# Performance work log

Measured on AMD Instinct MI355X. Metric: run time of the kernel, lower is better.

Reference implementation:

```python
import jax, jax.numpy as jnp
import numpy as np

B, N, C, H, E, K = 2, 2048, 1024, 4096, 8, 2
TAU = 1.0


def setup_inputs() -> dict:
    key = jax.random.key(0)
    ks = jax.random.split(key, 9)
    x = jax.random.normal(ks[0], (B, N, C), dtype=jnp.float32)
    T = B * N
    u = jax.random.uniform(ks[1], (T, E), minval=1e-6, maxval=1.0 - 1e-6)
    gumbel_noise = -jnp.log(-jnp.log(u))  # Gumbel(0,1) samples
    s = 0.02
    gate_w = jax.random.normal(ks[2], (C, E), dtype=jnp.float32) * s
    gate_b = jnp.zeros((E,), dtype=jnp.float32)
    w1 = jax.random.normal(ks[3], (E, C, H), dtype=jnp.float32) * s
    b1 = jnp.zeros((E, H), dtype=jnp.float32)
    w2 = jax.random.normal(ks[4], (E, H, C), dtype=jnp.float32) * s
    b2 = jnp.zeros((E, C), dtype=jnp.float32)
    return {"x": x, "gumbel_noise": gumbel_noise, "gate_w": gate_w,
            "gate_b": gate_b, "w1": w1, "b1": b1, "w2": w2, "b2": b2}


def reference(x, gumbel_noise, gate_w, gate_b, w1, b1, w2, b2):
    Bb, Nn, Cc = x.shape
    x_flat = x.reshape(-1, Cc)                                  # [T, C]
    logits = x_flat @ gate_w + gate_b                           # [T, E]
    # F.gumbel_softmax(hard=False, tau=1): softmax((logits + g)/tau)
    gates = jax.nn.softmax((logits + gumbel_noise) / TAU, axis=-1)
    mean_gates = gates.mean(axis=0)
    load_balance_loss = jnp.sum(mean_gates * jnp.log(mean_gates + 1e-8))
    topk_vals, topk_idxs = jax.lax.top_k(gates, K)              # [T, K]
    T = x_flat.shape[0]
    # scatter top-k gate weights into a dense [T, E] combine matrix
    comb = jnp.zeros((T, E), dtype=gates.dtype)
    comb = comb.at[jnp.arange(T)[:, None], topk_idxs].set(topk_vals)
    # dense per-expert MLP over all tokens, then weighted combine
    h = jnp.einsum('tc,ech->teh', x_flat, w1) + b1              # [T, E, H]
    h = jax.nn.gelu(h, approximate=False)                        # exact GELU (nn.GELU)
    y = jnp.einsum('teh,ehc->tec', h, w2) + b2                  # [T, E, C]
    out = jnp.einsum('te,tec->tc', comb, y)                     # [T, C]
    return out.reshape(Bb, Nn, Cc), load_balance_loss
```

## Files before the change

kernel.cpp:

```cpp
#include <hip/hip_runtime.h>
#include <math.h>

#define TT  4096
#define CC  1024
#define HH  4096
#define EE  8
#define TKN 8192

typedef _Float16 f16x8 __attribute__((ext_vector_type(8)));
typedef float    f32x4 __attribute__((ext_vector_type(4)));

#define GLD_LDS16(g, l)                                                        \
    __builtin_amdgcn_global_load_lds(                                          \
        (const __attribute__((address_space(1))) void*)(g),                    \
        (__attribute__((address_space(3))) void*)(l), 16, 0, 0)

__global__ __launch_bounds__(256) void gate_kernel(
    const float* __restrict__ x, const float* __restrict__ gn,
    const float* __restrict__ gw, const float* __restrict__ gb,
    int* __restrict__ topk_idx, float* __restrict__ topk_w,
    int* __restrict__ counts, float* __restrict__ gsum)
{
    int wave = threadIdx.x >> 6, lane = threadIdx.x & 63;
    int t = blockIdx.x * 4 + wave;
    const float* xrow = x + (size_t)t * CC;

    double acc[EE];
#pragma unroll
    for (int e = 0; e < EE; e++) acc[e] = 0.0;

#pragma unroll
    for (int i = 0; i < CC / 64; i++) {
        int c = i * 64 + lane;
        float xv = xrow[c];
        const float4* g4 = reinterpret_cast<const float4*>(gw + (size_t)c * EE);
        float4 g0 = g4[0], g1 = g4[1];
        double xd = (double)xv;
        acc[0] += xd * (double)g0.x; acc[1] += xd * (double)g0.y;
        acc[2] += xd * (double)g0.z; acc[3] += xd * (double)g0.w;
        acc[4] += xd * (double)g1.x; acc[5] += xd * (double)g1.y;
        acc[6] += xd * (double)g1.z; acc[7] += xd * (double)g1.w;
    }
#pragma unroll
    for (int e = 0; e < EE; e++)
#pragma unroll
        for (int off = 32; off > 0; off >>= 1)
            acc[e] += __shfl_xor(acc[e], off);

    double z[EE], m = -1e300;
#pragma unroll
    for (int e = 0; e < EE; e++) {
        z[e] = acc[e] + (double)gb[e] + (double)gn[(size_t)t * EE + e];
        m = fmax(m, z[e]);
    }
    double p[EE], s = 0.0;
#pragma unroll
    for (int e = 0; e < EE; e++) { p[e] = exp(z[e] - m); s += p[e]; }
    double inv = 1.0 / s;
    double g[EE];
#pragma unroll
    for (int e = 0; e < EE; e++) g[e] = p[e] * inv;

    int i1 = 0; double v1 = g[0];
#pragma unroll
    for (int e = 1; e < EE; e++) if (g[e] > v1) { v1 = g[e]; i1 = e; }
    int i2 = -1; double v2 = -1.0;
#pragma unroll
    for (int e = 0; e < EE; e++) if (e != i1 && g[e] > v2) { v2 = g[e]; i2 = e; }

    if (lane == 0) {
        topk_idx[t * 2 + 0] = i1; topk_w[t * 2 + 0] = (float)v1;
        topk_idx[t * 2 + 1] = i2; topk_w[t * 2 + 1] = (float)v2;
        atomicAdd(&counts[i1], 1);
        atomicAdd(&counts[i2], 1);
    }

    __shared__ float gp[4][EE];
    if (lane == 0) {
#pragma unroll
        for (int e = 0; e < EE; e++) gp[wave][e] = (float)g[e];
    }
    __syncthreads();
    if (threadIdx.x < EE) {
        float s4 = gp[0][threadIdx.x] + gp[1][threadIdx.x] +
                   gp[2][threadIdx.x] + gp[3][threadIdx.x];
        atomicAdd(&gsum[threadIdx.x], s4);
    }
}

__global__ __launch_bounds__(256) void transpose_f16_kernel(
    const float* __restrict__ src, _Float16* __restrict__ dst, int R, int Ccols)
{
    __shared__ float tile[64][65];
    int e = blockIdx.z;
    const float* s = src + (size_t)e * R * Ccols;
    _Float16* d = dst + (size_t)e * R * Ccols;
    int c0 = blockIdx.x * 64, r0 = blockIdx.y * 64;
    int tx = threadIdx.x, ty = threadIdx.y;
#pragma unroll
    for (int i = 0; i < 16; i++) {
        int r = ty + i * 4;
        tile[r][tx] = s[(size_t)(r0 + r) * Ccols + c0 + tx];
    }
    __syncthreads();
#pragma unroll
    for (int i = 0; i < 16; i++) {
        int c = ty + i * 4;
        d[(size_t)(c0 + c) * R + r0 + tx] = (_Float16)tile[tx][c];
    }
}

__global__ void scan_kernel(const int* __restrict__ counts, int* __restrict__ offsets,
                            const float* __restrict__ gsum, float* __restrict__ loss_out)
{
    if (threadIdx.x == 0) {
        int o = 0;
#pragma unroll
        for (int e = 0; e < EE; e++) { offsets[e] = o; o += counts[e]; }
        offsets[EE] = o;
        float L = 0.f;
#pragma unroll
        for (int e = 0; e < EE; e++) {
            float me = gsum[e] / (float)TT;
            L += me * logf(me + 1e-8f);
        }
        *loss_out = L;
    }
}

__global__ __launch_bounds__(256) void scatter_kernel(
    const int* __restrict__ topk_idx, const float* __restrict__ topk_w,
    const int* __restrict__ offsets, int* __restrict__ fill,
    int* __restrict__ rowtok, float* __restrict__ rweight)
{
    int t = blockIdx.x * 256 + threadIdx.x;
#pragma unroll
    for (int k = 0; k < 2; k++) {
        int e = topk_idx[t * 2 + k];
        int pos = offsets[e] + atomicAdd(&fill[e], 1);
        rowtok[pos] = t;
        rweight[pos] = topk_w[t * 2 + k];
    }
}

__global__ __launch_bounds__(256) void gather_kernel(
    const float* __restrict__ x, const int* __restrict__ rowtok,
    _Float16* __restrict__ xg)
{
    int p = blockIdx.x * 2 + (threadIdx.x >> 7);
    int c = (threadIdx.x & 127) * 8;
    int t = rowtok[p];
    const float4* s = reinterpret_cast<const float4*>(x + (size_t)t * CC + c);
    float4 v0 = s[0], v1 = s[1];
    f16x8 o;
    o[0] = (_Float16)v0.x; o[1] = (_Float16)v0.y;
    o[2] = (_Float16)v0.z; o[3] = (_Float16)v0.w;
    o[4] = (_Float16)v1.x; o[5] = (_Float16)v1.y;
    o[6] = (_Float16)v1.z; o[7] = (_Float16)v1.w;
    *reinterpret_cast<f16x8*>(xg + (size_t)p * CC + c) = o;
}

__global__ __launch_bounds__(256) void gemm1_kernel(
    const _Float16* __restrict__ xg, const _Float16* __restrict__ w1t,
    const float* __restrict__ b1, const int* __restrict__ offsets,
    _Float16* __restrict__ h)
{
    int e = blockIdx.z;
    int segs = offsets[e];
    int M = offsets[e + 1] - segs;
    int m0 = blockIdx.x * 128;
    if (m0 >= M) return;
    int n0 = blockIdx.y * 128;

    __shared__ __align__(16) _Float16 As[128][64];
    __shared__ __align__(16) _Float16 Bs[128][64];

    int tid = threadIdx.x;
    int wave = tid >> 6, lane = tid & 63;
    int wm = (wave >> 1) * 64, wn = (wave & 1) * 64;
    int lrow = lane & 15, kg = lane >> 4;

    const _Float16* wB = w1t + (size_t)e * HH * CC;

    const _Float16* ap[4]; const _Float16* bp[4];
    _Float16 *al[4], *bl[4];
#pragma unroll
    for (int j = 0; j < 4; j++) {
        int ch = (wave * 4 + j) * 64 + lane;
        int row = ch >> 3, kc = ch & 7;
        int rm = m0 + row; if (rm >= M) rm = M - 1;
        ap[j] = xg + (size_t)(segs + rm) * CC + kc * 8;
        bp[j] = wB + (size_t)(n0 + row) * CC + kc * 8;
        al[j] = &As[0][0] + ch * 8;
        bl[j] = &Bs[0][0] + ch * 8;
    }

    f32x4 acc[4][4];
#pragma unroll
    for (int i = 0; i < 4; i++)
#pragma unroll
        for (int j = 0; j < 4; j++)
#pragma unroll
            for (int r = 0; r < 4; r++) acc[i][j][r] = 0.f;

    for (int k0 = 0; k0 < CC; k0 += 64) {
#pragma unroll
        for (int j = 0; j < 4; j++) {
            GLD_LDS16(ap[j], al[j]);
            GLD_LDS16(bp[j], bl[j]);
            ap[j] += 64; bp[j] += 64;
        }
        __syncthreads();

        f16x8 aF[2][4], bF[2][4];
#pragma unroll
        for (int s = 0; s < 2; s++)
#pragma unroll
            for (int i = 0; i < 4; i++) {
                aF[s][i] = *reinterpret_cast<const f16x8*>(
                    &As[wm + i * 16 + lrow][s * 32 + kg * 8]);
                bF[s][i] = *reinterpret_cast<const f16x8*>(
                    &Bs[wn + i * 16 + lrow][s * 32 + kg * 8]);
            }
#pragma unroll
        for (int s = 0; s < 2; s++)
#pragma unroll
            for (int mi = 0; mi < 4; mi++)
#pragma unroll
                for (int ni = 0; ni < 4; ni++)
                    acc[mi][ni] = __builtin_amdgcn_mfma_f32_16x16x32_f16(
                        aF[s][mi], bF[s][ni], acc[mi][ni], 0, 0, 0);
        __syncthreads();
    }

    int rbase = (lane >> 4) * 4;
#pragma unroll
    for (int mi = 0; mi < 4; mi++) {
#pragma unroll
        for (int ni = 0; ni < 4; ni++) {
            int gcol = n0 + wn + ni * 16 + lrow;
            float bias = b1[(size_t)e * HH + gcol];
#pragma unroll
            for (int r = 0; r < 4; r++) {
                int rowl = m0 + wm + mi * 16 + rbase + r;
                if (rowl < M) {
                    float v = acc[mi][ni][r] + bias;
                    v = 0.5f * v * (1.0f + erff(v * 0.70710678118654752f));
                    h[(size_t)(segs + rowl) * HH + gcol] = (_Float16)v;
                }
            }
        }
    }
}

__global__ __launch_bounds__(256) void gemm2_kernel(
    const _Float16* __restrict__ h, const _Float16* __restrict__ w2t,
    const float* __restrict__ b2, const int* __restrict__ rowtok,
    const float* __restrict__ rweight, const int* __restrict__ offsets,
    float* __restrict__ out)
{
    int e = blockIdx.z;
    int segs = offsets[e];
    int M = offsets[e + 1] - segs;
    int m0 = blockIdx.x * 128;
    if (m0 >= M) return;
    int kz = blockIdx.y >> 3;
    int n0 = (blockIdx.y & 7) * 128;

    __shared__ __align__(16) _Float16 As[128][64];
    __shared__ __align__(16) _Float16 Bs[128][64];
    __shared__ int toks[128];
    __shared__ float wgt[128];

    int tid = threadIdx.x;
    if (tid < 128) {
        int r = m0 + tid;
        int rr = (r < M) ? r : (M - 1);
        toks[tid] = rowtok[segs + rr];
        wgt[tid] = rweight[segs + rr];
    }

    int wave = tid >> 6, lane = tid & 63;
    int wm = (wave >> 1) * 64, wn = (wave & 1) * 64;
    int lrow = lane & 15, kg = lane >> 4;

    const _Float16* wB = w2t + (size_t)e * CC * HH;
    int kbeg = kz * (HH / 2);

    const _Float16* ap[4]; const _Float16* bp[4];
    _Float16 *al[4], *bl[4];
#pragma unroll
    for (int j = 0; j < 4; j++) {
        int ch = (wave * 4 + j) * 64 + lane;
        int row = ch >> 3, kc = ch & 7;
        int rm = m0 + row; if (rm >= M) rm = M - 1;
        ap[j] = h  + (size_t)(segs + rm) * HH + kbeg + kc * 8;
        bp[j] = wB + (size_t)(n0 + row) * HH + kbeg + kc * 8;
        al[j] = &As[0][0] + ch * 8;
        bl[j] = &Bs[0][0] + ch * 8;
    }

    f32x4 acc[4][4];
#pragma unroll
    for (int i = 0; i < 4; i++)
#pragma unroll
        for (int j = 0; j < 4; j++)
#pragma unroll
            for (int r = 0; r < 4; r++) acc[i][j][r] = 0.f;

    for (int k0 = 0; k0 < HH / 2; k0 += 64) {
#pragma unroll
        for (int j = 0; j < 4; j++) {
            GLD_LDS16(ap[j], al[j]);
            GLD_LDS16(bp[j], bl[j]);
            ap[j] += 64; bp[j] += 64;
        }
        __syncthreads();

        f16x8 aF[2][4], bF[2][4];
#pragma unroll
        for (int s = 0; s < 2; s++)
#pragma unroll
            for (int i = 0; i < 4; i++) {
                aF[s][i] = *reinterpret_cast<const f16x8*>(
                    &As[wm + i * 16 + lrow][s * 32 + kg * 8]);
                bF[s][i] = *reinterpret_cast<const f16x8*>(
                    &Bs[wn + i * 16 + lrow][s * 32 + kg * 8]);
            }
#pragma unroll
        for (int s = 0; s < 2; s++)
#pragma unroll
            for (int mi = 0; mi < 4; mi++)
#pragma unroll
                for (int ni = 0; ni < 4; ni++)
                    acc[mi][ni] = __builtin_amdgcn_mfma_f32_16x16x32_f16(
                        aF[s][mi], bF[s][ni], acc[mi][ni], 0, 0, 0);
        __syncthreads();
    }

    int rbase = (lane >> 4) * 4;
#pragma unroll
    for (int mi = 0; mi < 4; mi++) {
#pragma unroll
        for (int ni = 0; ni < 4; ni++) {
            int gcol = n0 + wn + ni * 16 + lrow;
            float bias = (kz == 0) ? b2[(size_t)e * CC + gcol] : 0.f;
#pragma unroll
            for (int r = 0; r < 4; r++) {
                int rowl = m0 + wm + mi * 16 + rbase + r;
                if (rowl < M) {
                    int lr = rowl - m0;
                    float v = (acc[mi][ni][r] + bias) * wgt[lr];
                    unsafeAtomicAdd(&out[(size_t)toks[lr] * CC + gcol], v);
                }
            }
        }
    }
}

extern "C" void kernel_launch(void* const* d_in, const int* in_sizes, int n_in,
                              void* d_out, int out_size, void* d_ws, size_t ws_size,
                              hipStream_t stream)
{
    const float* x  = (const float*)d_in[0];
    const float* gn = (const float*)d_in[1];
    const float* gw = (const float*)d_in[2];
    const float* gb = (const float*)d_in[3];
    const float* w1 = (const float*)d_in[4];
    const float* b1 = (const float*)d_in[5];
    const float* w2 = (const float*)d_in[6];
    const float* b2 = (const float*)d_in[7];
    float* out = (float*)d_out;

    char* w = (char*)d_ws;
    int*   counts  = (int*)(w + 0);
    int*   fill    = (int*)(w + 32);
    int*   offsets = (int*)(w + 64);
    float* gsum    = (float*)(w + 128);
    size_t off = 256;
    int*   topk_idx = (int*)(w + off);   off += (size_t)TT * 2 * 4;
    float* topk_w   = (float*)(w + off); off += (size_t)TT * 2 * 4;
    int*   rowtok   = (int*)(w + off);   off += (size_t)TKN * 4;
    float* rweight  = (float*)(w + off); off += (size_t)TKN * 4;
    _Float16* xg  = (_Float16*)(w + off); off += (size_t)TKN * CC * 2;
    _Float16* w1t = (_Float16*)(w + off); off += (size_t)EE * HH * CC * 2;
    _Float16* w2t = (_Float16*)(w + off); off += (size_t)EE * CC * HH * 2;
    _Float16* hbuf = (_Float16*)(w + off); off += (size_t)TKN * HH * 2;

    (void)hipMemsetAsync(d_out, 0, (size_t)out_size * sizeof(float), stream);
    (void)hipMemsetAsync(d_ws, 0, 256, stream);

    gate_kernel<<<TT / 4, 256, 0, stream>>>(x, gn, gw, gb, topk_idx, topk_w,
                                            counts, gsum);
    transpose_f16_kernel<<<dim3(HH / 64, CC / 64, EE), dim3(64, 4), 0, stream>>>(
        w1, w1t, CC, HH);
    transpose_f16_kernel<<<dim3(CC / 64, HH / 64, EE), dim3(64, 4), 0, stream>>>(
        w2, w2t, HH, CC);
    scan_kernel<<<1, 64, 0, stream>>>(counts, offsets, gsum, out + (size_t)TT * CC);
    scatter_kernel<<<TT / 256, 256, 0, stream>>>(topk_idx, topk_w, offsets, fill,
                                                 rowtok, rweight);
    gather_kernel<<<TKN / 2, 256, 0, stream>>>(x, rowtok, xg);
    gemm1_kernel<<<dim3(12, HH / 128, EE), 256, 0, stream>>>(xg, w1t, b1,
                                                             offsets, hbuf);
    gemm2_kernel<<<dim3(12, 2 * (CC / 128), EE), 256, 0, stream>>>(
        hbuf, w2t, b2, rowtok, rweight, offsets, out);
}
```

Before: 909.2 us.

## Schedule expert GEMMs over a compact tile list with fixed-size grid

The scan kernel now builds compact lists of the valid (expert, n-tile, m-tile) work items for both expert GEMMs, plus their counts. The GEMM kernels launch a fixed grid of 768 blocks, and each block loops over a contiguous slice of that list. The aim is to stop launching many blocks that exit immediately because their m-tile lies past an expert's token count. Consecutive tiles in a block share the same expert and weight columns, which may improve L2 reuse. The cost is static partitioning in place of hardware block scheduling, which can leave tail imbalance, and more work in the single-block scan kernel.

```diff
diff --git a/kernel.cpp b/kernel.cpp
--- a/kernel.cpp
+++ b/kernel.cpp
@@ -6,6 +6,7 @@
 #define HH  4096
 #define EE  8
 #define TKN 8192
+#define PGRID 768
 
 typedef _Float16 f16x8 __attribute__((ext_vector_type(8)));
 typedef float    f32x4 __attribute__((ext_vector_type(4)));
@@ -110,14 +111,24 @@
     }
 }
 
-__global__ void scan_kernel(const int* __restrict__ counts, int* __restrict__ offsets,
-                            const float* __restrict__ gsum, float* __restrict__ loss_out)
-{
-    if (threadIdx.x == 0) {
-        int o = 0;
-#pragma unroll
-        for (int e = 0; e < EE; e++) { offsets[e] = o; o += counts[e]; }
+__global__ __launch_bounds__(256) void scan_kernel(
+    const int* __restrict__ counts, int* __restrict__ offsets,
+    const float* __restrict__ gsum, float* __restrict__ loss_out,
+    int* __restrict__ tiles1, int* __restrict__ tiles2, int* __restrict__ ntl)
+{
+    __shared__ int s_mt[EE], s_tb1[EE], s_tb2[EE];
+    int tid = threadIdx.x;
+    if (tid == 0) {
+        int o = 0, t1 = 0, t2 = 0;
+#pragma unroll
+        for (int e = 0; e < EE; e++) {
+            offsets[e] = o;
+            int mt = (counts[e] + 127) >> 7;
+            s_mt[e] = mt; s_tb1[e] = t1; s_tb2[e] = t2;
+            o += counts[e]; t1 += mt * (HH / 128); t2 += mt * 2 * (CC / 128);
+        }
         offsets[EE] = o;
+        ntl[0] = t1; ntl[1] = t2;
         float L = 0.f;
 #pragma unroll
         for (int e = 0; e < EE; e++) {
@@ -125,6 +136,19 @@
             L += me * logf(me + 1e-8f);
         }
         *loss_out = L;
+    }
+    __syncthreads();
+    {
+        int e = tid >> 5, n = tid & 31;
+        int base = s_tb1[e] + n * s_mt[e];
+        for (int m = 0; m < s_mt[e]; m++)
+            tiles1[base + m] = (e << 20) | (n << 12) | m;
+    }
+    if (tid < 128) {
+        int e = tid >> 4, nk = tid & 15;
+        int base = s_tb2[e] + nk * s_mt[e];
+        for (int m = 0; m < s_mt[e]; m++)
+            tiles2[base + m] = (e << 20) | (nk << 12) | m;
     }
 }
 
@@ -163,90 +187,96 @@
 __global__ __launch_bounds__(256) void gemm1_kernel(
     const _Float16* __restrict__ xg, const _Float16* __restrict__ w1t,
     const float* __restrict__ b1, const int* __restrict__ offsets,
+    const int* __restrict__ tiles, const int* __restrict__ ntl,
     _Float16* __restrict__ h)
 {
-    int e = blockIdx.z;
-    int segs = offsets[e];
-    int M = offsets[e + 1] - segs;
-    int m0 = blockIdx.x * 128;
-    if (m0 >= M) return;
-    int n0 = blockIdx.y * 128;
-
     __shared__ __align__(16) _Float16 As[128][64];
     __shared__ __align__(16) _Float16 Bs[128][64];
+
+    int nt = ntl[0];
+    int q = (nt + PGRID - 1) / PGRID;
+    int t0 = blockIdx.x * q;
+    int t1 = t0 + q; if (t1 > nt) t1 = nt;
 
     int tid = threadIdx.x;
     int wave = tid >> 6, lane = tid & 63;
     int wm = (wave >> 1) * 64, wn = (wave & 1) * 64;
     int lrow = lane & 15, kg = lane >> 4;
-
-    const _Float16* wB = w1t + (size_t)e * HH * CC;
-
-    const _Float16* ap[4]; const _Float16* bp[4];
-    _Float16 *al[4], *bl[4];
-#pragma unroll
-    for (int j = 0; j < 4; j++) {
-        int ch = (wave * 4 + j) * 64 + lane;
-        int row = ch >> 3, kc = ch & 7;
-        int rm = m0 + row; if (rm >= M) rm = M - 1;
-        ap[j] = xg + (size_t)(segs + rm) * CC + kc * 8;
-        bp[j] = wB + (size_t)(n0 + row) * CC + kc * 8;
-        al[j] = &As[0][0] + ch * 8;
-        bl[j] = &Bs[0][0] + ch * 8;
-    }
-
-    f32x4 acc[4][4];
-#pragma unroll
-    for (int i = 0; i < 4; i++)
-#pragma unroll
-        for (int j = 0; j < 4; j++)
-#pragma unroll
-            for (int r = 0; r < 4; r++) acc[i][j][r] = 0.f;
-
-    for (int k0 = 0; k0 < CC; k0 += 64) {
+    int ch0 = wave * 4 * 64 + lane;
+    int rbase = (lane >> 4) * 4;
+
+    for (int ti = t0; ti < t1; ti++) {
+        int id = tiles[ti];
+        int e = id >> 20, n0 = ((id >> 12) & 0xFF) * 128, m0 = (id & 0xFFF) * 128;
+        int segs = offsets[e];
+        int M = offsets[e + 1] - segs;
+        const _Float16* wB = w1t + (size_t)e * HH * CC;
+
+        const _Float16* ap[4]; const _Float16* bp[4];
+        _Float16 *al[4], *bl[4];
 #pragma unroll
         for (int j = 0; j < 4; j++) {
-            GLD_LDS16(ap[j], al[j]);
-            GLD_LDS16(bp[j], bl[j]);
-            ap[j] += 64; bp[j] += 64;
-        }
-        __syncthreads();
-
-        f16x8 aF[2][4], bF[2][4];
-#pragma unroll
-        for (int s = 0; s < 2; s++)
-#pragma unroll
-            for (int i = 0; i < 4; i++) {
-                aF[s][i] = *reinterpret_cast<const f16x8*>(
-                    &As[wm + i * 16 + lrow][s * 32 + kg * 8]);
-                bF[s][i] = *reinterpret_cast<const f16x8*>(
-                    &Bs[wn + i * 16 + lrow][s * 32 + kg * 8]);
+            int ch = ch0 + j * 64;
+            int row = ch >> 3, kc = ch & 7;
+            int rm = m0 + row; if (rm >= M) rm = M - 1;
+            ap[j] = xg + (size_t)(segs + rm) * CC + kc * 8;
+            bp[j] = wB + (size_t)(n0 + row) * CC + kc * 8;
+            al[j] = &As[0][0] + ch * 8;
+            bl[j] = &Bs[0][0] + ch * 8;
+        }
+
+        f32x4 acc[4][4];
+#pragma unroll
+        for (int i = 0; i < 4; i++)
+#pragma unroll
+            for (int j = 0; j < 4; j++)
+#pragma unroll
+                for (int r = 0; r < 4; r++) acc[i][j][r] = 0.f;
+
+        for (int k0 = 0; k0 < CC; k0 += 64) {
+#pragma unroll
+            for (int j = 0; j < 4; j++) {
+                GLD_LDS16(ap[j], al[j]);
+                GLD_LDS16(bp[j], bl[j]);
+                ap[j] += 64; bp[j] += 64;
             }
-#pragma unroll
-        for (int s = 0; s < 2; s++)
-#pragma unroll
-            for (int mi = 0; mi < 4; mi++)
-#pragma unroll
-                for (int ni = 0; ni < 4; ni++)
-                    acc[mi][ni] = __builtin_amdgcn_mfma_f32_16x16x32_f16(
-                        aF[s][mi], bF[s][ni], acc[mi][ni], 0, 0, 0);
-        __syncthreads();
-    }
-
-    int rbase = (lane >> 4) * 4;
-#pragma unroll
-    for (int mi = 0; mi < 4; mi++) {
-#pragma unroll
-        for (int ni = 0; ni < 4; ni++) {
-            int gcol = n0 + wn + ni * 16 + lrow;
-            float bias = b1[(size_t)e * HH + gcol];
-#pragma unroll
-            for (int r = 0; r < 4; r++) {
-                int rowl = m0 + wm + mi * 16 + rbase + r;
-                if (rowl < M) {
-                    float v = acc[mi][ni][r] + bias;
-                    v = 0.5f * v * (1.0f + erff(v * 0.70710678118654752f));
-                    h[(size_t)(segs + rowl) * HH + gcol] = (_Float16)v;
+            __syncthreads();
+
+            f16x8 aF[2][4], bF[2][4];
+#pragma unroll
+            for (int s = 0; s < 2; s++)
+#pragma unroll
+                for (int i = 0; i < 4; i++) {
+                    aF[s][i] = *reinterpret_cast<const f16x8*>(
+                        &As[wm + i * 16 + lrow][s * 32 + kg * 8]);
+                    bF[s][i] = *reinterpret_cast<const f16x8*>(
+                        &Bs[wn + i * 16 + lrow][s * 32 + kg * 8]);
+                }
+#pragma unroll
+            for (int s = 0; s < 2; s++)
+#pragma unroll
+                for (int mi = 0; mi < 4; mi++)
+#pragma unroll
+                    for (int ni = 0; ni < 4; ni++)
+                        acc[mi][ni] = __builtin_amdgcn_mfma_f32_16x16x32_f16(
+                            aF[s][mi], bF[s][ni], acc[mi][ni], 0, 0, 0);
+            __syncthreads();
+        }
+
+#pragma unroll
+        for (int mi = 0; mi < 4; mi++) {
+#pragma unroll
+            for (int ni = 0; ni < 4; ni++) {
+                int gcol = n0 + wn + ni * 16 + lrow;
+                float bias = b1[(size_t)e * HH + gcol];
+#pragma unroll
+                for (int r = 0; r < 4; r++) {
+                    int rowl = m0 + wm + mi * 16 + rbase + r;
+                    if (rowl < M) {
+                        float v = acc[mi][ni][r] + bias;
+                        v = 0.5f * v * (1.0f + erff(v * 0.70710678118654752f));
+                        h[(size_t)(segs + rowl) * HH + gcol] = (_Float16)v;
+                    }
                 }
             }
         }
@@ -257,101 +287,108 @@
     const _Float16* __restrict__ h, const _Float16* __restrict__ w2t,
     const float* __restrict__ b2, const int* __restrict__ rowtok,
     const float* __restrict__ rweight, const int* __restrict__ offsets,
+    const int* __restrict__ tiles, const int* __restrict__ ntl,
     float* __restrict__ out)
 {
-    int e = blockIdx.z;
-    int segs = offsets[e];
-    int M = offsets[e + 1] - segs;
-    int m0 = blockIdx.x * 128;
-    if (m0 >= M) return;
-    int kz = blockIdx.y >> 3;
-    int n0 = (blockIdx.y & 7) * 128;
-
     __shared__ __align__(16) _Float16 As[128][64];
     __shared__ __align__(16) _Float16 Bs[128][64];
     __shared__ int toks[128];
     __shared__ float wgt[128];
 
+    int nt = ntl[1];
+    int q = (nt + PGRID - 1) / PGRID;
+    int t0 = blockIdx.x * q;
+    int t1 = t0 + q; if (t1 > nt) t1 = nt;
+
     int tid = threadIdx.x;
-    if (tid < 128) {
-        int r = m0 + tid;
-        int rr = (r < M) ? r : (M - 1);
-        toks[tid] = rowtok[segs + rr];
-        wgt[tid] = rweight[segs + rr];
-    }
-
     int wave = tid >> 6, lane = tid & 63;
     int wm = (wave >> 1) * 64, wn = (wave & 1) * 64;
     int lrow = lane & 15, kg = lane >> 4;
-
-    const _Float16* wB = w2t + (size_t)e * CC * HH;
-    int kbeg = kz * (HH / 2);
-
-    const _Float16* ap[4]; const _Float16* bp[4];
-    _Float16 *al[4], *bl[4];
-#pragma unroll
-    for (int j = 0; j < 4; j++) {
-        int ch = (wave * 4 + j) * 64 + lane;
-        int row = ch >> 3, kc = ch & 7;
-        int rm = m0 + row; if (rm >= M) rm = M - 1;
-        ap[j] = h  + (size_t)(segs + rm) * HH + kbeg + kc * 8;
-        bp[j] = wB + (size_t)(n0 + row) * HH + kbeg + kc * 8;
-        al[j] = &As[0][0] + ch * 8;
-        bl[j] = &Bs[0][0] + ch * 8;
-    }
-
-    f32x4 acc[4][4];
-#pragma unroll
-    for (int i = 0; i < 4; i++)
-#pragma unroll
-        for (int j = 0; j < 4; j++)
-#pragma unroll
-            for (int r = 0; r < 4; r++) acc[i][j][r] = 0.f;
-
-    for (int k0 = 0; k0 < HH / 2; k0 += 64) {
+    int ch0 = wave * 4 * 64 + lane;
+    int rbase = (lane >> 4) * 4;
+
+    for (int ti = t0; ti < t1; ti++) {
+        int id = tiles[ti];
+        int e = id >> 20, nk = (id >> 12) & 0xFF, m0 = (id & 0xFFF) * 128;
+        int kz = nk >> 3, n0 = (nk & 7) * 128;
+        int segs = offsets[e];
+        int M = offsets[e + 1] - segs;
+        const _Float16* wB = w2t + (size_t)e * CC * HH;
+        int kbeg = kz * (HH / 2);
+
+        __syncthreads();
+        if (tid < 128) {
+            int r = m0 + tid;
+            int rr = (r < M) ? r : (M - 1);
+            toks[tid] = rowtok[segs + rr];
+            wgt[tid] = rweight[segs + rr];
+        }
+
+        const _Float16* ap[4]; const _Float16* bp[4];
+        _Float16 *al[4], *bl[4];
 #pragma unroll
         for (int j = 0; j < 4; j++) {
-            GLD_LDS16(ap[j], al[j]);
-            GLD_LDS16(bp[j], bl[j]);
-            ap[j] += 64; bp[j] += 64;
-        }
-        __syncthreads();
-
-        f16x8 aF[2][4], bF[2][4];
-#pragma unroll
-        for (int s = 0; s < 2; s++)
-#pragma unroll
-            for (int i = 0; i < 4; i++) {
-                aF[s][i] = *reinterpret_cast<const f16x8*>(
-                    &As[wm + i * 16 + lrow][s * 32 + kg * 8]);
-                bF[s][i] = *reinterpret_cast<const f16x8*>(
-                    &Bs[wn + i * 16 + lrow][s * 32 + kg * 8]);
+            int ch = ch0 + j * 64;
+            int row = ch >> 3, kc = ch & 7;
+            int rm = m0 + row; if (rm >= M) rm = M - 1;
+            ap[j] = h  + (size_t)(segs + rm) * HH + kbeg + kc * 8;
+            bp[j] = wB + (size_t)(n0 + row) * HH + kbeg + kc * 8;
+            al[j] = &As[0][0] + ch * 8;
+            bl[j] = &Bs[0][0] + ch * 8;
+        }
+
+        f32x4 acc[4][4];
+#pragma unroll
+        for (int i = 0; i < 4; i++)
+#pragma unroll
+            for (int j = 0; j < 4; j++)
+#pragma unroll
+                for (int r = 0; r < 4; r++) acc[i][j][r] = 0.f;
+
+        for (int k0 = 0; k0 < HH / 2; k0 += 64) {
+#pragma unroll
+            for (int j = 0; j < 4; j++) {
+                GLD_LDS16(ap[j], al[j]);
+                GLD_LDS16(bp[j], bl[j]);
+                ap[j] += 64; bp[j] += 64;
             }
-#pragma unroll
-        for (int s = 0; s < 2; s++)
-#pragma unroll
-            for (int mi = 0; mi < 4; mi++)
-#pragma unroll
-                for (int ni = 0; ni < 4; ni++)
-                    acc[mi][ni] = __builtin_amdgcn_mfma_f32_16x16x32_f16(
-                        aF[s][mi], bF[s][ni], acc[mi][ni], 0, 0, 0);
-        __syncthreads();
-    }
-
-    int rbase = (lane >> 4) * 4;
-#pragma unroll
-    for (int mi = 0; mi < 4; mi++) {
-#pragma unroll
-        for (int ni = 0; ni < 4; ni++) {
-            int gcol = n0 + wn + ni * 16 + lrow;
-            float bias = (kz == 0) ? b2[(size_t)e * CC + gcol] : 0.f;
-#pragma unroll
-            for (int r = 0; r < 4; r++) {
-                int rowl = m0 + wm + mi * 16 + rbase + r;
-                if (rowl < M) {
-                    int lr = rowl - m0;
-                    float v = (acc[mi][ni][r] + bias) * wgt[lr];
-                    unsafeAtomicAdd(&out[(size_t)toks[lr] * CC + gcol], v);
+            __syncthreads();
+
+            f16x8 aF[2][4], bF[2][4];
+#pragma unroll
+            for (int s = 0; s < 2; s++)
+#pragma unroll
+                for (int i = 0; i < 4; i++) {
+                    aF[s][i] = *reinterpret_cast<const f16x8*>(
+                        &As[wm + i * 16 + lrow][s * 32 + kg * 8]);
+                    bF[s][i] = *reinterpret_cast<const f16x8*>(
+                        &Bs[wn + i * 16 + lrow][s * 32 + kg * 8]);
+                }
+#pragma unroll
+            for (int s = 0; s < 2; s++)
+#pragma unroll
+                for (int mi = 0; mi < 4; mi++)
+#pragma unroll
+                    for (int ni = 0; ni < 4; ni++)
+                        acc[mi][ni] = __builtin_amdgcn_mfma_f32_16x16x32_f16(
+                            aF[s][mi], bF[s][ni], acc[mi][ni], 0, 0, 0);
+            __syncthreads();
+        }
+
+#pragma unroll
+        for (int mi = 0; mi < 4; mi++) {
+#pragma unroll
+            for (int ni = 0; ni < 4; ni++) {
+                int gcol = n0 + wn + ni * 16 + lrow;
+                float bias = (kz == 0) ? b2[(size_t)e * CC + gcol] : 0.f;
+#pragma unroll
+                for (int r = 0; r < 4; r++) {
+                    int rowl = m0 + wm + mi * 16 + rbase + r;
+                    if (rowl < M) {
+                        int lr = rowl - m0;
+                        float v = (acc[mi][ni][r] + bias) * wgt[lr];
+                        unsafeAtomicAdd(&out[(size_t)toks[lr] * CC + gcol], v);
+                    }
                 }
             }
         }
@@ -377,11 +414,14 @@
     int*   fill    = (int*)(w + 32);
     int*   offsets = (int*)(w + 64);
     float* gsum    = (float*)(w + 128);
+    int*   ntl     = (int*)(w + 192);
     size_t off = 256;
     int*   topk_idx = (int*)(w + off);   off += (size_t)TT * 2 * 4;
     float* topk_w   = (float*)(w + off); off += (size_t)TT * 2 * 4;
     int*   rowtok   = (int*)(w + off);   off += (size_t)TKN * 4;
     float* rweight  = (float*)(w + off); off += (size_t)TKN * 4;
+    int*   tiles1   = (int*)(w + off);   off += 4096 * 4;
+    int*   tiles2   = (int*)(w + off);   off += 2048 * 4;
     _Float16* xg  = (_Float16*)(w + off); off += (size_t)TKN * CC * 2;
     _Float16* w1t = (_Float16*)(w + off); off += (size_t)EE * HH * CC * 2;
     _Float16* w2t = (_Float16*)(w + off); off += (size_t)EE * CC * HH * 2;
@@ -396,12 +436,12 @@
         w1, w1t, CC, HH);
     transpose_f16_kernel<<<dim3(CC / 64, HH / 64, EE), dim3(64, 4), 0, stream>>>(
         w2, w2t, HH, CC);
-    scan_kernel<<<1, 64, 0, stream>>>(counts, offsets, gsum, out + (size_t)TT * CC);
+    scan_kernel<<<1, 256, 0, stream>>>(counts, offsets, gsum,
+                                       out + (size_t)TT * CC, tiles1, tiles2, ntl);
     scatter_kernel<<<TT / 256, 256, 0, stream>>>(topk_idx, topk_w, offsets, fill,
                                                  rowtok, rweight);
     gather_kernel<<<TKN / 2, 256, 0, stream>>>(x, rowtok, xg);
-    gemm1_kernel<<<dim3(12, HH / 128, EE), 256, 0, stream>>>(xg, w1t, b1,
-                                                             offsets, hbuf);
-    gemm2_kernel<<<dim3(12, 2 * (CC / 128), EE), 256, 0, stream>>>(
-        hbuf, w2t, b2, rowtok, rweight, offsets, out);
-}
+    gemm1_kernel<<<PGRID, 256, 0, stream>>>(xg, w1t, b1, offsets, tiles1, ntl, hbuf);
+    gemm2_kernel<<<PGRID, 256, 0, stream>>>(hbuf, w2t, b2, rowtok, rweight,
+                                            offsets, tiles2, ntl, out);
+}
```

Result: slower. 976.9 us (+7.4%).
